# Optimization experiments

Hardware: AMD Instinct MI355X
Metric: run time of the kernel (lower is better)

Reference implementation:

```python
import jax, jax.numpy as jnp
import numpy as np

B, D, H = 4096, 64, 1024  # batch, state dim, hidden width


def setup_inputs() -> dict:
    key = jax.random.key(0)
    ks = jax.random.split(key, 4)
    def w(k, shape, fan_in):
        return (jax.random.normal(k, shape, jnp.float32) / np.float32(np.sqrt(fan_in)))
    return {
        "x": jax.random.normal(ks[0], (B, 1 + D), jnp.float32),
        "W1": w(ks[1], (D, H), D),
        "b1": jnp.zeros((H,), jnp.float32),
        "W2": w(ks[2], (H, H), H),
        "b2": jnp.zeros((H,), jnp.float32),
        "W3": w(ks[3], (H, D), H),
        "b3": jnp.zeros((D,), jnp.float32),
    }


def _mlp(z, W1, b1, W2, b2, W3, b3):
    # tanh MLP vector field: d -> h -> h -> d
    h = jnp.tanh(z @ W1 + b1)
    h = jnp.tanh(h @ W2 + b2)
    return h @ W3 + b3


def reference(x, W1, b1, W2, b2, W3, b3):
    x_in = x[:, 1:]                        # [B, D] state (col 0 is logp channel)
    f = lambda z: _mlp(z, W1, b1, W2, b2, W3, b3)
    x_out = f(x_in)                        # [B, D]

    # Exact Jacobian trace: same math as the torch per-dim autograd.grad loop,
    # expressed as D forward-mode JVPs vmapped over the identity basis.
    eye = jnp.eye(x_in.shape[1], dtype=x.dtype)

    def diag_entry(e):                     # e: [D] basis vector
        _, t = jax.jvp(f, (x_in,), (jnp.broadcast_to(e, x_in.shape),))
        return t @ e                       # [B] = J[:, i, i]

    trJ = jnp.sum(jax.vmap(diag_entry)(eye), axis=0)  # [B]

    out = jnp.concatenate([-trJ[:, None], x_out], axis=1)  # [B, 1+D]
    return out + 0.0 * x  # faithful to `+ 0 * x` in the original
```

## Files before the change

kernel.cpp:

```cpp
#include <hip/hip_runtime.h>
#include <cmath>

typedef unsigned short u16;
typedef __attribute__((ext_vector_type(8))) short s8v;
typedef __attribute__((ext_vector_type(4))) float f4v;
typedef __attribute__((ext_vector_type(16))) float f16v;

__device__ __forceinline__ u16 f2bf(float f) {
    union { float f; unsigned u; } v; v.f = f;
    unsigned r = v.u + 0x7FFFu + ((v.u >> 16) & 1u);
    return (u16)(r >> 16);
}
__device__ __forceinline__ float tanh_fast(float x) {
    float e = __builtin_amdgcn_exp2f(x * 2.88539008177792681f);
    return 1.f - 2.f * __builtin_amdgcn_rcpf(1.f + e);
}
__device__ __forceinline__ int wslot(int row, int c) {
    return ((((c >> 2) << 6) | ((c & 3) << 4) | (row & 15)) ^ c);
}
__device__ __forceinline__ size_t fragoff(int n, int k) {
    return (((size_t)(n >> 5) * 64 + (k >> 4)) * 64 + (n & 31) + (((k >> 3) & 1) << 5)) * 8 + (k & 7);
}

__launch_bounds__(256)
__global__ void cnf_prep(const float* __restrict__ x, const float* __restrict__ W1,
                         const float* __restrict__ W2, const float* __restrict__ W3,
                         u16* __restrict__ W2Tf, u16* __restrict__ VTf,
                         u16* __restrict__ xb, u16* __restrict__ W1T,
                         u16* __restrict__ W3Tf, float* __restrict__ trJ)
{
    __shared__ float w2s[32][33];
    __shared__ __align__(16) float w1s[64][36];
    const int a = blockIdx.x * 32;
    const int b = blockIdx.y * 32;
    const int t = threadIdx.x;

    #pragma unroll
    for (int it = 0; it < 4; ++it) {
        int idx = t + it * 256;
        w2s[idx >> 5][idx & 31] = W2[(a + (idx >> 5)) * 1024 + b + (idx & 31)];
    }
    #pragma unroll
    for (int it = 0; it < 8; ++it) {
        int idx = t + it * 256;
        w1s[idx >> 5][idx & 31] = W1[(idx >> 5) * 1024 + a + (idx & 31)];
    }
    __syncthreads();

    #pragma unroll
    for (int it = 0; it < 4; ++it) {
        int idx = t + it * 256;
        int rr = idx >> 5, cc = idx & 31;
        W2Tf[fragoff(b + rr, a + cc)] = f2bf(w2s[cc][rr]);
    }
    {
        const int q = t >> 3, pg = t & 7;
        const float* w3row = W3 + (b + q) * 64;
        f4v u = f4v{0.f, 0.f, 0.f, 0.f};
        #pragma unroll
        for (int i4 = 0; i4 < 16; ++i4) {
            f4v w3v = *(const f4v*)&w3row[i4 * 4];
            #pragma unroll
            for (int s = 0; s < 4; ++s) {
                f4v wv = *(const f4v*)&w1s[i4 * 4 + s][pg * 4];
                u += w3v[s] * wv;
            }
        }
        #pragma unroll
        for (int j = 0; j < 4; ++j) {
            const int pp = pg * 4 + j;
            VTf[fragoff(b + q, a + pp)] = f2bf(w2s[pp][q] * u[j]);
        }
    }
    {
        int bid = blockIdx.y * 32 + blockIdx.x;
        int e = bid * 256 + t;
        xb[e] = f2bf(x[(e >> 6) * 65 + 1 + (e & 63)]);
    }
    if (blockIdx.y == 0) {
        int pp = t >> 3, i0 = (t & 7) * 8;
        s8v v;
        #pragma unroll
        for (int j = 0; j < 8; ++j) v[j] = (short)f2bf(w1s[i0 + j][pp]);
        *(s8v*)&W1T[(a + pp) * 64 + i0] = v;
        if (t < 128) trJ[blockIdx.x * 128 + t] = 0.f;
    }
    if (blockIdx.y == 1) {
        int idx = blockIdx.x * 256 + t;
        int n = idx & 63, k0 = (idx >> 6) * 8;
        s8v v;
        #pragma unroll
        for (int j = 0; j < 8; ++j) v[j] = (short)f2bf(W3[(k0 + j) * 64 + n]);
        *(s8v*)&W3Tf[fragoff(n, k0)] = v;
    }
}

__launch_bounds__(256)
__global__ void cnf_gemm1(const u16* __restrict__ xb, const u16* __restrict__ W1T,
                          const float* __restrict__ b1,
                          u16* __restrict__ h1f, u16* __restrict__ g1f)
{
    __shared__ __align__(16) u16 lds[12 * 1024];
    __shared__ __align__(16) u16 hls[128 * 64];
    __shared__ __align__(16) u16 gls[128 * 64];
    const int t = threadIdx.x;
    const int wave = t >> 6, lane = t & 63;
    const int wm = wave >> 1, wn = wave & 1;
    const int g = lane >> 4, lr = lane & 15;
    const int arow0 = blockIdx.x * 128, bcol0 = blockIdx.y * 64;

    #pragma unroll
    for (int i = 0; i < 4; ++i) {
        int ch = t + i * 256, row = ch >> 3, c = ch & 7;
        *(s8v*)&lds[(row >> 4) * 1024 + wslot(row, c) * 8] =
            *(const s8v*)&xb[(arow0 + row) * 64 + c * 8];
    }
    #pragma unroll
    for (int i = 0; i < 2; ++i) {
        int ch = t + i * 256, row = ch >> 3, c = ch & 7;
        *(s8v*)&lds[(8 + (row >> 4)) * 1024 + wslot(row, c) * 8] =
            *(const s8v*)&W1T[(bcol0 + row) * 64 + c * 8];
    }
    __syncthreads();

    f4v acc[4][2];
    #pragma unroll
    for (int mi = 0; mi < 4; ++mi)
        #pragma unroll
        for (int ni = 0; ni < 2; ++ni) acc[mi][ni] = f4v{0.f,0.f,0.f,0.f};

    #pragma unroll
    for (int ks = 0; ks < 2; ++ks) {
        const int lo = (ks * 64 + (lane ^ ((ks * 4 + g) & 7))) * 8;
        s8v af[4], bf[2];
        #pragma unroll
        for (int mi = 0; mi < 4; ++mi) af[mi] = *(const s8v*)&lds[(wm * 4 + mi) * 1024 + lo];
        #pragma unroll
        for (int ni = 0; ni < 2; ++ni) bf[ni] = *(const s8v*)&lds[(8 + wn * 2 + ni) * 1024 + lo];
        #pragma unroll
        for (int mi = 0; mi < 4; ++mi)
            #pragma unroll
            for (int ni = 0; ni < 2; ++ni)
                acc[mi][ni] = __builtin_amdgcn_mfma_f32_16x16x32_bf16(af[mi], bf[ni], acc[mi][ni], 0, 0, 0);
    }

    #pragma unroll
    for (int mi = 0; mi < 4; ++mi) {
        const int rowl = wm * 64 + mi * 16 + g * 4;
        #pragma unroll
        for (int ni = 0; ni < 2; ++ni) {
            const int coll = wn * 32 + ni * 16 + lr;
            const float bv = b1[bcol0 + coll];
            const int cc = coll >> 3, jj = coll & 7;
            #pragma unroll
            for (int r = 0; r < 4; ++r) {
                const int row = rowl + r;
                float h = tanh_fast(acc[mi][ni][r] + bv);
                int idx = row * 64 + ((cc ^ (row & 7)) << 3) + jj;
                hls[idx] = f2bf(h);
                gls[idx] = f2bf(1.f - h * h);
            }
        }
    }
    __syncthreads();

    const int rt0 = arow0 >> 5, kk0 = bcol0 >> 4;
    #pragma unroll
    for (int i = 0; i < 4; ++i) {
        const int tile = (i * 256 + t) >> 6;
        const int ln = t & 63;
        const int rt = tile >> 2, kk = tile & 3;
        const int row = rt * 32 + (ln & 31);
        const int kb = kk * 16 + (ln >> 5) * 8;
        const int src = row * 64 + (((kb >> 3) ^ (row & 7)) << 3);
        const size_t dst = ((size_t)(rt0 + rt) * 64 + (kk0 + kk)) * 512 + ln * 8;
        *(s8v*)&h1f[dst] = *(const s8v*)&hls[src];
        *(s8v*)&g1f[dst] = *(const s8v*)&gls[src];
    }
}

#define LOADB(B, kt)                                                           \
    do { _Pragma("unroll")                                                     \
         for (int _ks = 0; _ks < 2; ++_ks) {                                   \
             size_t _o = (((size_t)(ntb + wn) * 64 + (kt) * 2 + _ks) * 512) + lane * 8; \
             B[_ks*2 + 0] = *(const s8v*)&W2Tf[_o];                            \
             B[_ks*2 + 1] = *(const s8v*)&VTf[_o];                             \
         } } while (0)

#define MIDBODY(kt, AwH, AwG, AlH, AlG, Bc, Bn)                                \
    {                                                                          \
        const u16* _buf = &lds[(kt) & 1][0];                                   \
        s8v a1[2][2], a2[2][2];                                  \
        _Pragma("unroll")                                                      \
        for (int ks = 0; ks < 2; ++ks)                                         \
            _Pragma("unroll")                                                  \
            for (int mt = 0; mt < 2; ++mt) {                                   \
                const int f = ((wrt * 2 + mt) * 2 + ks) * 512 + lane * 8;      \
                a1[ks][mt] = *(const s8v*)&_buf[f];                            \
                a2[ks][mt] = *(const s8v*)&_buf[4096 + f];                     \
            }                                                                  \
        if ((kt) < 30) {                                                       \
            const size_t _go = (size_t)((kt) + 2) * 1024;                      \
            AlH[0] = *(const s8v*)(h1f + sg0 + _go);                           \
            AlH[1] = *(const s8v*)(h1f + sg1 + _go);                           \
            AlG[0] = *(const s8v*)(g1f + sg0 + _go);                           \
            AlG[1] = *(const s8v*)(g1f + sg1 + _go);                           \
        }                                                                      \
        if ((kt) < 31) {                                                       \
            u16* _wb = &lds[((kt) + 1) & 1][0];                                \
            *(s8v*)&_wb[sd0] = AwH[0];        *(s8v*)&_wb[sd1] = AwH[1];       \
            *(s8v*)&_wb[4096 + sd0] = AwG[0]; *(s8v*)&_wb[4096 + sd1] = AwG[1];\
            LOADB(Bn, (kt) + 1);                                               \
        }                                                                      \
        _Pragma("unroll")                                                      \
        for (int ks = 0; ks < 2; ++ks)                                         \
            _Pragma("unroll")                                                  \
            for (int mt = 0; mt < 2; ++mt) {                                   \
                acc1[mt] = __builtin_amdgcn_mfma_f32_32x32x16_bf16(a1[ks][mt], Bc[ks*2+0], acc1[mt], 0, 0, 0); \
                acc2[mt] = __builtin_amdgcn_mfma_f32_32x32x16_bf16(a2[ks][mt], Bc[ks*2+1], acc2[mt], 0, 0, 0); \
            }                                                                  \
        __syncthreads();                                                       \
    }

__launch_bounds__(256)
__global__ void cnf_mid(const u16* __restrict__ h1f, const u16* __restrict__ g1f,
                        const u16* __restrict__ W2Tf, const u16* __restrict__ VTf,
                        const float* __restrict__ b2,
                        u16* __restrict__ h2f, float* __restrict__ trJ)
{
    __shared__ __align__(16) u16 lds[2][8192];

    const int t = threadIdx.x;
    const int wave = t >> 6, lane = t & 63;
    const int wrt = wave & 1;
    const int wn  = wave >> 1;
    const int bx = blockIdx.x;
    const int by = blockIdx.y;
    const int arow0 = bx * 128;
    const int ntb = by * 2;

    const int lc8 = (t & 63) * 8;
    const int c0rt = t >> 7, c0kk = (t >> 6) & 1;
    const size_t sg0 = ((size_t)(bx * 4 + c0rt) * 64 + c0kk) * 512 + lc8;
    const size_t sg1 = ((size_t)(bx * 4 + 2 + c0rt) * 64 + c0kk) * 512 + lc8;
    const int sd0 = (c0rt * 2 + c0kk) * 512 + lc8;
    const int sd1 = ((2 + c0rt) * 2 + c0kk) * 512 + lc8;

    f16v acc1[2], acc2[2];
    #pragma unroll
    for (int mt = 0; mt < 2; ++mt)
        #pragma unroll
        for (int r = 0; r < 16; ++r) { acc1[mt][r] = 0.f; acc2[mt][r] = 0.f; }

    s8v raH[2], raG[2], rbH[2], rbG[2];
    s8v bA[4], bB[4];

    raH[0] = *(const s8v*)(h1f + sg0); raH[1] = *(const s8v*)(h1f + sg1);
    raG[0] = *(const s8v*)(g1f + sg0); raG[1] = *(const s8v*)(g1f + sg1);
    {
        u16* wb = &lds[0][0];
        *(s8v*)&wb[sd0] = raH[0];        *(s8v*)&wb[sd1] = raH[1];
        *(s8v*)&wb[4096 + sd0] = raG[0]; *(s8v*)&wb[4096 + sd1] = raG[1];
    }
    raH[0] = *(const s8v*)(h1f + sg0 + 1024); raH[1] = *(const s8v*)(h1f + sg1 + 1024);
    raG[0] = *(const s8v*)(g1f + sg0 + 1024); raG[1] = *(const s8v*)(g1f + sg1 + 1024);
    LOADB(bA, 0);
    __syncthreads();

    for (int kt2 = 0; kt2 < 16; ++kt2) {
        const int kt = kt2 * 2;
        MIDBODY(kt,     raH, raG, rbH, rbG, bA, bB);
        MIDBODY(kt + 1, rbH, rbG, raH, raG, bB, bA);
    }

    const int l31 = lane & 31, lh = lane >> 5;
    #pragma unroll
    for (int mt = 0; mt < 2; ++mt) {
        const int rt = (arow0 >> 5) + wrt * 2 + mt;
        const int q0 = (ntb + wn) * 32;
        const float bv = b2[q0 + l31];
        const size_t hb = (((size_t)rt * 64 + ((q0 + l31) >> 4)) * 64
                           + (((l31 >> 3) & 1) << 5)) * 8 + (l31 & 7) + lh * 32;
        float tr[16];
        #pragma unroll
        for (int r = 0; r < 16; ++r) {
            float hh = tanh_fast(acc1[mt][r] + bv);
            float gg = 1.f - hh * hh;
            h2f[hb + ((r & 3) + ((r >> 2) << 3)) * 8] = f2bf(hh);
            tr[r] = acc2[mt][r] * gg;
        }
        #pragma unroll
        for (int off = 1; off < 32; off <<= 1)
            #pragma unroll
            for (int r = 0; r < 16; ++r) tr[r] += __shfl_xor(tr[r], off);
        if (l31 == 0) {
            const int rowb = arow0 + (wrt * 2 + mt) * 32 + lh * 4;
            #pragma unroll
            for (int r = 0; r < 16; ++r)
                atomicAdd(&trJ[rowb + (r & 3) + ((r >> 2) << 3)], tr[r]);
        }
    }
}

__launch_bounds__(256)
__global__ void cnf_out(const u16* __restrict__ h2f, const u16* __restrict__ W3Tf,
                        const float* __restrict__ b3, const float* __restrict__ trJ,
                        float* __restrict__ out)
{
    __shared__ float red[4][32][32];
    const int t = threadIdx.x;
    const int wave = t >> 6, lane = t & 63;
    const int rt = blockIdx.x;
    const int nb = blockIdx.y;

    f16v acc;
    #pragma unroll
    for (int r = 0; r < 16; ++r) acc[r] = 0.f;

    #pragma unroll
    for (int kki = 0; kki < 16; ++kki) {
        const int kk = wave * 16 + kki;
        s8v af = *(const s8v*)&h2f[(((size_t)rt * 64 + kk) * 64 + lane) * 8];
        s8v bf = *(const s8v*)&W3Tf[(((size_t)nb * 64 + kk) * 64 + lane) * 8];
        acc = __builtin_amdgcn_mfma_f32_32x32x16_bf16(af, bf, acc, 0, 0, 0);
    }
    const int l31 = lane & 31, lh = lane >> 5;
    #pragma unroll
    for (int r = 0; r < 16; ++r)
        red[wave][(r & 3) + ((r >> 2) << 3) + lh * 4][l31] = acc[r];
    __syncthreads();

    #pragma unroll
    for (int i = 0; i < 4; ++i) {
        int o = t + i * 256;
        int row = o >> 5, col = o & 31;
        float s = red[0][row][col] + red[1][row][col] + red[2][row][col]
                + red[3][row][col] + b3[nb * 32 + col];
        out[(size_t)(rt * 32 + row) * 65 + 1 + nb * 32 + col] = s;
    }
    if (nb == 0 && t < 32) out[(size_t)(rt * 32 + t) * 65] = -trJ[rt * 32 + t];
}

extern "C" void kernel_launch(void* const* d_in, const int* in_sizes, int n_in,
                              void* d_out, int out_size, void* d_ws, size_t ws_size,
                              hipStream_t stream) {
    const float* x  = (const float*)d_in[0];
    const float* W1 = (const float*)d_in[1];
    const float* b1 = (const float*)d_in[2];
    const float* W2 = (const float*)d_in[3];
    const float* b2 = (const float*)d_in[4];
    const float* W3 = (const float*)d_in[5];
    const float* b3 = (const float*)d_in[6];
    float* out = (float*)d_out;

    char* ws = (char*)d_ws;
    u16*   h1f = (u16*)(ws);
    u16*   g1f = (u16*)(ws + (size_t)( 8u << 20));
    u16*   h2f = (u16*)(ws + (size_t)(16u << 20));
    u16*   W2T = (u16*)(ws + (size_t)(24u << 20));
    u16*   VTb = (u16*)(ws + (size_t)(26u << 20));
    float* trJ = (float*)(ws + (size_t)(28u << 20));
    u16*   xbb = (u16*)(ws + (size_t)(28u << 20) + 65536);
    u16*   W1T = (u16*)(ws + (size_t)(28u << 20) + 65536 + 524288);
    u16*   W3T = (u16*)(ws + (size_t)(28u << 20) + 65536 + 524288 + 131072);

    cnf_prep <<<dim3(32, 32), 256, 0, stream>>>(x, W1, W2, W3, W2T, VTb, xbb, W1T, W3T, trJ);
    cnf_gemm1<<<dim3(32, 16), 256, 0, stream>>>(xbb, W1T, b1, h1f, g1f);
    cnf_mid  <<<dim3(32, 16), 256, 0, stream>>>(h1f, g1f, W2T, VTb, b2, h2f, trJ);
    cnf_out  <<<dim3(128, 2), 256, 0, stream>>>(h2f, W3T, b3, trJ, out);
}
```

Baseline: 56.19 us.

## Widen cnf_mid blocks to 512 threads and remap grid for L2 locality

The mid GEMM kernel now runs 512-thread blocks (8 waves) covering 4 N-tiles instead of 2, so each block loads its A tile (h1/g1) once and shares it across twice as many waves. Each thread now stages half as much A data per k-step. The 2D grid is flattened to 256 blocks with a swizzled mapping that groups row-blocks, aiming at better L2 reuse and fewer A-tile reloads. The trade-off is fewer blocks (one per CU on a 256-CU part), and launch_bounds(512,1) limits occupancy.

```diff
diff --git a/kernel.cpp b/kernel.cpp
--- a/kernel.cpp
+++ b/kernel.cpp
@@ -201,15 +201,12 @@
             }                                                                  \
         if ((kt) < 30) {                                                       \
             const size_t _go = (size_t)((kt) + 2) * 1024;                      \
-            AlH[0] = *(const s8v*)(h1f + sg0 + _go);                           \
-            AlH[1] = *(const s8v*)(h1f + sg1 + _go);                           \
-            AlG[0] = *(const s8v*)(g1f + sg0 + _go);                           \
-            AlG[1] = *(const s8v*)(g1f + sg1 + _go);                           \
+            AlH = *(const s8v*)(h1f + sg0 + _go);                              \
+            AlG = *(const s8v*)(g1f + sg0 + _go);                              \
         }                                                                      \
         if ((kt) < 31) {                                                       \
             u16* _wb = &lds[((kt) + 1) & 1][0];                                \
-            *(s8v*)&_wb[sd0] = AwH[0];        *(s8v*)&_wb[sd1] = AwH[1];       \
-            *(s8v*)&_wb[4096 + sd0] = AwG[0]; *(s8v*)&_wb[4096 + sd1] = AwG[1];\
+            *(s8v*)&_wb[sd0] = AwH; *(s8v*)&_wb[4096 + sd0] = AwG;             \
             LOADB(Bn, (kt) + 1);                                               \
         }                                                                      \
         _Pragma("unroll")                                                      \
@@ -222,7 +219,7 @@
         __syncthreads();                                                       \
     }
 
-__launch_bounds__(256)
+__launch_bounds__(512, 1)
 __global__ void cnf_mid(const u16* __restrict__ h1f, const u16* __restrict__ g1f,
                         const u16* __restrict__ W2Tf, const u16* __restrict__ VTf,
                         const float* __restrict__ b2,
@@ -234,17 +231,17 @@
     const int wave = t >> 6, lane = t & 63;
     const int wrt = wave & 1;
     const int wn  = wave >> 1;
-    const int bx = blockIdx.x;
-    const int by = blockIdx.y;
+    const int bid = blockIdx.x;
+    const int k8 = bid & 7, j = bid >> 3;
+    const int bx = k8 * 4 + (j & 3);
+    const int by = j >> 2;
     const int arow0 = bx * 128;
-    const int ntb = by * 2;
+    const int ntb = by * 4;
 
     const int lc8 = (t & 63) * 8;
-    const int c0rt = t >> 7, c0kk = (t >> 6) & 1;
-    const size_t sg0 = ((size_t)(bx * 4 + c0rt) * 64 + c0kk) * 512 + lc8;
-    const size_t sg1 = ((size_t)(bx * 4 + 2 + c0rt) * 64 + c0kk) * 512 + lc8;
-    const int sd0 = (c0rt * 2 + c0kk) * 512 + lc8;
-    const int sd1 = ((2 + c0rt) * 2 + c0kk) * 512 + lc8;
+    const int rt_s = t >> 7, kk_s = (t >> 6) & 1;
+    const size_t sg0 = ((size_t)(bx * 4 + rt_s) * 64 + kk_s) * 512 + lc8;
+    const int sd0 = (rt_s * 2 + kk_s) * 512 + lc8;
 
     f16v acc1[2], acc2[2];
     #pragma unroll
@@ -252,18 +249,17 @@
         #pragma unroll
         for (int r = 0; r < 16; ++r) { acc1[mt][r] = 0.f; acc2[mt][r] = 0.f; }
 
-    s8v raH[2], raG[2], rbH[2], rbG[2];
+    s8v raH, raG, rbH, rbG;
     s8v bA[4], bB[4];
 
-    raH[0] = *(const s8v*)(h1f + sg0); raH[1] = *(const s8v*)(h1f + sg1);
-    raG[0] = *(const s8v*)(g1f + sg0); raG[1] = *(const s8v*)(g1f + sg1);
+    raH = *(const s8v*)(h1f + sg0);
+    raG = *(const s8v*)(g1f + sg0);
     {
         u16* wb = &lds[0][0];
-        *(s8v*)&wb[sd0] = raH[0];        *(s8v*)&wb[sd1] = raH[1];
-        *(s8v*)&wb[4096 + sd0] = raG[0]; *(s8v*)&wb[4096 + sd1] = raG[1];
-    }
-    raH[0] = *(const s8v*)(h1f + sg0 + 1024); raH[1] = *(const s8v*)(h1f + sg1 + 1024);
-    raG[0] = *(const s8v*)(g1f + sg0 + 1024); raG[1] = *(const s8v*)(g1f + sg1 + 1024);
+        *(s8v*)&wb[sd0] = raH; *(s8v*)&wb[4096 + sd0] = raG;
+    }
+    raH = *(const s8v*)(h1f + sg0 + 1024);
+    raG = *(const s8v*)(g1f + sg0 + 1024);
     LOADB(bA, 0);
     __syncthreads();
 
@@ -366,6 +362,6 @@
 
     cnf_prep <<<dim3(32, 32), 256, 0, stream>>>(x, W1, W2, W3, W2T, VTb, xbb, W1T, W3T, trJ);
     cnf_gemm1<<<dim3(32, 16), 256, 0, stream>>>(xbb, W1T, b1, h1f, g1f);
-    cnf_mid  <<<dim3(32, 16), 256, 0, stream>>>(h1f, g1f, W2T, VTb, b2, h2f, trJ);
+    cnf_mid  <<<256,          512, 0, stream>>>(h1f, g1f, W2T, VTb, b2, h2f, trJ);
     cnf_out  <<<dim3(128, 2), 256, 0, stream>>>(h2f, W3T, b3, trJ, out);
 }
```

Result: no change. 56.77 us (+1.0%).
